# Optimization experiments

Measured on AMD Instinct MI355X. Metric: run time of the kernel, lower is better.

Reference implementation:

```python
import jax, jax.numpy as jnp
import numpy as np
import math

B_SZ, T, D_IN, D_OUT, N = 8, 4096, 128, 128, 256
MAX_PHASE, RMIN, RMAX = math.pi, 0.0, 1.0


def setup_inputs() -> dict:
    key = jax.random.key(0)
    ks = jax.random.split(key, 9)
    x = jax.random.normal(ks[0], (B_SZ, T, D_IN), dtype=jnp.float32)
    # lambda parameterization exactly as in LRU.__init__
    u1 = jax.random.uniform(ks[1], (N,), minval=1e-4, maxval=1.0)
    u2 = jax.random.uniform(ks[2], (N,), minval=1e-4, maxval=1.0)
    nu_log = jnp.log(-0.5 * jnp.log(u1 * (RMAX + RMIN) * (RMAX - RMIN) + RMIN ** 2))
    theta_log = jnp.log(MAX_PHASE * u2)
    lam_abs = jnp.exp(-jnp.exp(nu_log))
    gamma_log = jnp.log(jnp.sqrt(1.0 - jnp.square(lam_abs)))
    B_re = jax.random.normal(ks[3], (N, D_IN)) / math.sqrt(2 * D_IN)
    B_im = jax.random.normal(ks[4], (N, D_IN)) / math.sqrt(2 * D_IN)
    C_re = jax.random.normal(ks[5], (D_OUT, N)) / math.sqrt(N)
    C_im = jax.random.normal(ks[6], (D_OUT, N)) / math.sqrt(N)
    D = jax.random.normal(ks[7], (D_OUT, D_IN)) / math.sqrt(D_IN)
    return {"x": x, "nu_log": nu_log, "theta_log": theta_log, "gamma_log": gamma_log,
            "B_re": B_re, "B_im": B_im, "C_re": C_re, "C_im": C_im, "D": D}


def _binary_op_diag(e1, e2):
    a1, b1 = e1
    a2, b2 = e2
    return a1 * a2, a2 * b1 + b2


def reference(x, nu_log, theta_log, gamma_log, B_re, B_im, C_re, C_im, D):
    # ss_params()
    lam_abs = jnp.exp(-jnp.exp(nu_log))
    phase = jnp.exp(theta_log)
    lam = (lam_abs * jnp.cos(phase) + 1j * (lam_abs * jnp.sin(phase))).astype(jnp.complex64)  # [N]
    gammas = jnp.exp(gamma_log)[:, None]
    Bc = (gammas * (B_re + 1j * B_im)).astype(jnp.complex64)  # [N, D_IN]
    Cc = (C_re + 1j * C_im).astype(jnp.complex64)             # [D_OUT, N]
    # diagonal complex linear recurrence via associative scan over time
    Bu = x.astype(Bc.dtype) @ Bc.T                            # [B, T, N] complex
    lam_el = jnp.broadcast_to(lam, Bu.shape)                  # [B, T, N]
    _, states = jax.lax.associative_scan(_binary_op_diag, (lam_el, Bu), axis=1)
    y = jnp.real(states @ Cc.T) + x @ D.T                     # [B, T, D_OUT]
    return y
```

## Files before the change

### kernel.cpp

```cpp
#include <hip/hip_runtime.h>
#include <math.h>

#define B_SZ 8
#define T_LEN 4096
#define D_IN 128
#define D_OUT 128
#define N_ST 256
#define BT (B_SZ * T_LEN)
#define CHUNK 64
#define NCHUNK (T_LEN / CHUNK)
#define NBLK (B_SZ * NCHUNK)

typedef __attribute__((ext_vector_type(8))) short short8;
typedef __attribute__((ext_vector_type(4))) float f32x4;
typedef unsigned int uint;
typedef unsigned short ushort;

static __device__ __forceinline__ short f2bf(float f) {
  union { float f; uint u; } v; v.f = f;
  uint r = v.u + 0x7FFFu + ((v.u >> 16) & 1u);
  return (short)(r >> 16);
}
static __device__ __forceinline__ float bf2f(uint h) {
  union { uint u; float f; } v; v.u = h << 16;
  return v.f;
}
static __device__ __forceinline__ uint pack2(float a, float b) {
  return (uint)(ushort)f2bf(a) | ((uint)(ushort)f2bf(b) << 16);
}

__global__ __launch_bounds__(256) void k0_setup(
    const float* __restrict__ x,
    const float* __restrict__ nu_log, const float* __restrict__ theta_log,
    const float* __restrict__ gamma_log,
    const float* __restrict__ B_re, const float* __restrict__ B_im,
    const float* __restrict__ C_re, const float* __restrict__ C_im,
    const float* __restrict__ Dm,
    short* __restrict__ Wf1, short* __restrict__ Wf2,
    float2* __restrict__ lampow2, short* __restrict__ xbf) {
  int blk = blockIdx.x;
  if (blk < 320) {
    int idx = blk * 256 + threadIdx.x;
    if (idx < 16 * 512 * 8) {
      int j = idx & 7, col = (idx >> 3) & 511, kg = idx >> 12;
      int k = kg * 8 + j;
      int n = col >> 1, ri = col & 1;
      float g = expf(gamma_log[n]);
      float v = g * (ri ? B_im[n * D_IN + k] : B_re[n * D_IN + k]);
      Wf1[idx] = f2bf(v);
    }
    if (idx < 80 * 128 * 8) {
      int j = idx & 7, d = (idx >> 3) & 127, kg = idx >> 10;
      int k = kg * 8 + j;
      float v;
      if (k < 512) {
        int n = k >> 1;
        v = (k & 1) ? -C_im[d * N_ST + n] : C_re[d * N_ST + n];
      } else {
        v = Dm[d * D_IN + (k - 512)];
      }
      Wf2[idx] = f2bf(v);
    }
  } else if (blk < 385) {
    int j = blk - 320;
    int n = threadIdx.x;
    float e_nu = expf(nu_log[n]);
    float phase = expf(theta_log[n]);
    float r = expf(-(float)j * e_nu);
    float a = (float)j * phase;
    float2 v; v.x = r * cosf(a); v.y = r * sinf(a);
    lampow2[j * N_ST + n] = v;
  } else {
    size_t i = (size_t)(blk - 385) * 256 + threadIdx.x;
    const float4* x4 = (const float4*)x;
    float4 a = x4[2 * i], b = x4[2 * i + 1];
    uint4 u;
    u.x = pack2(a.x, a.y); u.y = pack2(a.z, a.w);
    u.z = pack2(b.x, b.y); u.w = pack2(b.z, b.w);
    ((uint4*)xbf)[i] = u;
  }
}

__global__ __launch_bounds__(256, 2) void kA(
    const short* __restrict__ xbf, const short* __restrict__ Wf1,
    const float2* __restrict__ lampow2,
    uint* __restrict__ states, float2* __restrict__ E) {
  __shared__ short bu[64 * 520];

  int bc = blockIdx.x;
  size_t row0 = (size_t)bc * CHUNK;
  int tid = threadIdx.x;
  int lane = tid & 63, w = tid >> 6;
  int m = lane & 15, q = lane >> 4;

  f32x4 acc[32];
#pragma unroll
  for (int ct = 0; ct < 32; ++ct) acc[ct] = (f32x4){0.f, 0.f, 0.f, 0.f};

  const short* xrow = xbf + (row0 + 16 * w + m) * D_IN;

  for (int ks = 0; ks < 4; ++ks) {
    short8 af = *(const short8*)(xrow + 32 * ks + 8 * q);
    const short* wbase = Wf1 + ((size_t)(4 * ks + q) * 512 + m) * 8;
#pragma unroll
    for (int ct = 0; ct < 32; ++ct) {
      short8 bf = *(const short8*)(wbase + 16 * ct * 8);
      acc[ct] = __builtin_amdgcn_mfma_f32_16x16x32_bf16(af, bf, acc[ct], 0, 0, 0);
    }
  }

#pragma unroll
  for (int ct = 0; ct < 32; ++ct) {
#pragma unroll
    for (int r = 0; r < 4; ++r) {
      bu[(16 * w + 4 * q + r) * 520 + 16 * ct + m] = f2bf(acc[ct][r]);
    }
  }
  __syncthreads();

  int n = tid;
  float2 lam = lampow2[N_ST + n];
  float sre = 0.f, sim = 0.f;
  uint* sg = states + row0 * N_ST + n;
  for (int j = 0; j < CHUNK; ++j) {
    uint p = ((const uint*)(bu + j * 520))[n];
    float br = bf2f(p & 0xffffu), bi = bf2f(p >> 16);
    float nr = fmaf(lam.x, sre, fmaf(-lam.y, sim, br));
    float ni = fmaf(lam.x, sim, fmaf(lam.y, sre, bi));
    sre = nr; sim = ni;
    sg[(size_t)j * N_ST] = pack2(sre, sim);
  }
  float2 e; e.x = sre; e.y = sim;
  E[bc * N_ST + n] = e;
}

__global__ __launch_bounds__(256) void kB(
    const float2* __restrict__ E, const float2* __restrict__ lampow2,
    float2* __restrict__ P) {
  __shared__ float2 Es[NCHUNK * N_ST];

  int b = blockIdx.x;
  int tid = threadIdx.x;

  const float4* src = (const float4*)(E + (size_t)b * NCHUNK * N_ST);
  float4* dst = (float4*)Es;
#pragma unroll
  for (int it = 0; it < (NCHUNK * N_ST / 2) / 256; ++it) {
    dst[it * 256 + tid] = src[it * 256 + tid];
  }
  __syncthreads();

  int n = tid;
  float2 lamL = lampow2[CHUNK * N_ST + n];
  float cre = 0.f, cim = 0.f;
  for (int c = 0; c < NCHUNK; ++c) {
    size_t i = ((size_t)b * NCHUNK + c) * N_ST + n;
    float2 pv; pv.x = cre; pv.y = cim;
    P[i] = pv;
    float2 e = Es[c * N_ST + n];
    float nre = fmaf(lamL.x, cre, fmaf(-lamL.y, cim, e.x));
    float nim = fmaf(lamL.x, cim, fmaf(lamL.y, cre, e.y));
    cre = nre; cim = nim;
  }
}

__global__ __launch_bounds__(256, 4) void kC(
    const short* __restrict__ xbf, const uint* __restrict__ states,
    const float2* __restrict__ P, const float2* __restrict__ lampow2,
    const short* __restrict__ Wf2, float* __restrict__ y) {
  __shared__ short As[32 * 640];

  int blk = blockIdx.x;
  int bc = blk >> 1;
  int j0 = (blk & 1) * 32;
  size_t row0 = (size_t)blk * 32;
  int tid = threadIdx.x;
  int n4 = tid & 63, rblk = tid >> 6;

  float4 pA = *(const float4*)(P + (size_t)bc * N_ST + 4 * n4);
  float4 pB = *(const float4*)(P + (size_t)bc * N_ST + 4 * n4 + 2);

  {
    int kxp = tid & 63, r0 = tid >> 6;
    int k = 512 + 2 * kxp;
    int g = k >> 3, koff = k & 7;
    for (int rr = 0; rr < 8; ++rr) {
      int row = r0 * 8 + rr;
      uint xv = *(const uint*)(xbf + (row0 + row) * D_IN + 2 * kxp);
      int gp = (g & ~7) | ((g + row) & 7);
      *(uint*)(As + row * 640 + gp * 8 + koff) = xv;
    }
  }

  {
#pragma unroll
    for (int rr = 0; rr < 8; ++rr) {
      int row = rblk * 8 + rr;
      int j = j0 + row;
      uint4 sp = *(const uint4*)(states + ((row0 + row) * N_ST + 4 * n4));
      float4 lpa = *(const float4*)(lampow2 + ((size_t)(j + 1) * N_ST + 4 * n4));
      float4 lpb = *(const float4*)(lampow2 + ((size_t)(j + 1) * N_ST + 4 * n4 + 2));
      uint4 outv;
      {
        float sr = bf2f(sp.x & 0xffffu) + lpa.x * pA.x - lpa.y * pA.y;
        float si = bf2f(sp.x >> 16)     + lpa.x * pA.y + lpa.y * pA.x;
        outv.x = pack2(sr, si);
      }
      {
        float sr = bf2f(sp.y & 0xffffu) + lpa.z * pA.z - lpa.w * pA.w;
        float si = bf2f(sp.y >> 16)     + lpa.z * pA.w + lpa.w * pA.z;
        outv.y = pack2(sr, si);
      }
      {
        float sr = bf2f(sp.z & 0xffffu) + lpb.x * pB.x - lpb.y * pB.y;
        float si = bf2f(sp.z >> 16)     + lpb.x * pB.y + lpb.y * pB.x;
        outv.z = pack2(sr, si);
      }
      {
        float sr = bf2f(sp.w & 0xffffu) + lpb.z * pB.z - lpb.w * pB.w;
        float si = bf2f(sp.w >> 16)     + lpb.z * pB.w + lpb.w * pB.z;
        outv.w = pack2(sr, si);
      }
      int g = n4;
      int gp = (g & ~7) | ((g + row) & 7);
      *(uint4*)(As + row * 640 + gp * 8) = outv;
    }
  }
  __syncthreads();

  int lane = tid & 63, w = tid >> 6;
  int m = lane & 15, q = lane >> 4;

  f32x4 acc[2][2];
#pragma unroll
  for (int rt = 0; rt < 2; ++rt)
#pragma unroll
    for (int ci = 0; ci < 2; ++ci) acc[rt][ci] = (f32x4){0.f, 0.f, 0.f, 0.f};

  for (int ks = 0; ks < 20; ++ks) {
    int g = 4 * ks + q;
    int gp = (g & ~7) | ((g + m) & 7);
    short8 af0 = *(const short8*)(As + m * 640 + gp * 8);
    short8 af1 = *(const short8*)(As + (16 + m) * 640 + gp * 8);
    const short* wbase = Wf2 + ((size_t)g * 128 + m) * 8;
#pragma unroll
    for (int ci = 0; ci < 2; ++ci) {
      int ctg = 2 * w + ci;
      short8 bf = *(const short8*)(wbase + 16 * ctg * 8);
      acc[0][ci] = __builtin_amdgcn_mfma_f32_16x16x32_bf16(af0, bf, acc[0][ci], 0, 0, 0);
      acc[1][ci] = __builtin_amdgcn_mfma_f32_16x16x32_bf16(af1, bf, acc[1][ci], 0, 0, 0);
    }
  }

#pragma unroll
  for (int ci = 0; ci < 2; ++ci) {
    int ctg = 2 * w + ci;
#pragma unroll
    for (int rt = 0; rt < 2; ++rt) {
#pragma unroll
      for (int r = 0; r < 4; ++r) {
        y[(row0 + 16 * rt + 4 * q + r) * D_OUT + 16 * ctg + m] = acc[rt][ci][r];
      }
    }
  }
}

extern "C" void kernel_launch(void* const* d_in, const int* in_sizes, int n_in,
                              void* d_out, int out_size, void* d_ws, size_t ws_size,
                              hipStream_t stream) {
  const float* x         = (const float*)d_in[0];
  const float* nu_log    = (const float*)d_in[1];
  const float* theta_log = (const float*)d_in[2];
  const float* gamma_log = (const float*)d_in[3];
  const float* B_re      = (const float*)d_in[4];
  const float* B_im      = (const float*)d_in[5];
  const float* C_re      = (const float*)d_in[6];
  const float* C_im      = (const float*)d_in[7];
  const float* Dm        = (const float*)d_in[8];
  float* y = (float*)d_out;

  char* wp = (char*)d_ws;
  float2* lampow2 = (float2*)wp; wp += (size_t)(CHUNK + 1) * N_ST * sizeof(float2);
  short*  Wf1     = (short*)wp;  wp += (size_t)16 * 512 * 8 * sizeof(short);
  short*  Wf2     = (short*)wp;  wp += (size_t)80 * 128 * 8 * sizeof(short);
  float2* E       = (float2*)wp; wp += (size_t)NBLK * N_ST * sizeof(float2);
  float2* P       = (float2*)wp; wp += (size_t)NBLK * N_ST * sizeof(float2);
  short*  xbf     = (short*)wp;  wp += (size_t)BT * D_IN * sizeof(short);
  uint*   states  = (uint*)wp;   wp += (size_t)BT * N_ST * sizeof(uint);

  hipLaunchKernelGGL(k0_setup, dim3(385 + BT * D_IN / 8 / 256), dim3(256), 0, stream,
                     x, nu_log, theta_log, gamma_log, B_re, B_im, C_re, C_im,
                     Dm, Wf1, Wf2, lampow2, xbf);
  hipLaunchKernelGGL(kA, dim3(NBLK), dim3(256), 0, stream,
                     xbf, Wf1, lampow2, states, E);
  hipLaunchKernelGGL(kB, dim3(B_SZ), dim3(256), 0, stream,
                     E, lampow2, P);
  hipLaunchKernelGGL(kC, dim3(2 * NBLK), dim3(256), 0, stream,
                     xbf, states, P, lampow2, Wf2, y);
}
```

Before: 129.6 us.

## Recompute chunk-local scan in output kernel instead of storing states

```diff
diff --git a/kernel.cpp b/kernel.cpp
--- a/kernel.cpp
+++ b/kernel.cpp
@@ -83,8 +83,7 @@
 
 __global__ __launch_bounds__(256, 2) void kA(
     const short* __restrict__ xbf, const short* __restrict__ Wf1,
-    const float2* __restrict__ lampow2,
-    uint* __restrict__ states, float2* __restrict__ E) {
+    const float2* __restrict__ lampow2, float2* __restrict__ E) {
   __shared__ short bu[64 * 520];
 
   int bc = blockIdx.x;
@@ -121,14 +120,12 @@
   int n = tid;
   float2 lam = lampow2[N_ST + n];
   float sre = 0.f, sim = 0.f;
-  uint* sg = states + row0 * N_ST + n;
   for (int j = 0; j < CHUNK; ++j) {
     uint p = ((const uint*)(bu + j * 520))[n];
     float br = bf2f(p & 0xffffu), bi = bf2f(p >> 16);
     float nr = fmaf(lam.x, sre, fmaf(-lam.y, sim, br));
     float ni = fmaf(lam.x, sim, fmaf(lam.y, sre, bi));
     sre = nr; sim = ni;
-    sg[(size_t)j * N_ST] = pack2(sre, sim);
   }
   float2 e; e.x = sre; e.y = sim;
   E[bc * N_ST + n] = e;
@@ -164,102 +161,110 @@
   }
 }
 
-__global__ __launch_bounds__(256, 4) void kC(
-    const short* __restrict__ xbf, const uint* __restrict__ states,
+__global__ __launch_bounds__(256, 1) void kC(
+    const short* __restrict__ xbf, const short* __restrict__ Wf1,
     const float2* __restrict__ P, const float2* __restrict__ lampow2,
     const short* __restrict__ Wf2, float* __restrict__ y) {
-  __shared__ short As[32 * 640];
-
-  int blk = blockIdx.x;
-  int bc = blk >> 1;
-  int j0 = (blk & 1) * 32;
-  size_t row0 = (size_t)blk * 32;
+  __shared__ short bu[64 * 520];
+  __shared__ short As[64 * 640];
+
+  int bc = blockIdx.x;
+  size_t row0 = (size_t)bc * CHUNK;
   int tid = threadIdx.x;
-  int n4 = tid & 63, rblk = tid >> 6;
-
-  float4 pA = *(const float4*)(P + (size_t)bc * N_ST + 4 * n4);
-  float4 pB = *(const float4*)(P + (size_t)bc * N_ST + 4 * n4 + 2);
+  int lane = tid & 63, w = tid >> 6;
+  int m = lane & 15, q = lane >> 4;
+
+  f32x4 acc[32];
+#pragma unroll
+  for (int ct = 0; ct < 32; ++ct) acc[ct] = (f32x4){0.f, 0.f, 0.f, 0.f};
+
+  const short* xrow = xbf + (row0 + 16 * w + m) * D_IN;
+
+  for (int ks = 0; ks < 4; ++ks) {
+    short8 af = *(const short8*)(xrow + 32 * ks + 8 * q);
+    const short* wbase = Wf1 + ((size_t)(4 * ks + q) * 512 + m) * 8;
+#pragma unroll
+    for (int ct = 0; ct < 32; ++ct) {
+      short8 bf = *(const short8*)(wbase + 16 * ct * 8);
+      acc[ct] = __builtin_amdgcn_mfma_f32_16x16x32_bf16(af, bf, acc[ct], 0, 0, 0);
+    }
+  }
+
+#pragma unroll
+  for (int ct = 0; ct < 32; ++ct) {
+#pragma unroll
+    for (int r = 0; r < 4; ++r) {
+      bu[(16 * w + 4 * q + r) * 520 + 16 * ct + m] = f2bf(acc[ct][r]);
+    }
+  }
 
   {
     int kxp = tid & 63, r0 = tid >> 6;
     int k = 512 + 2 * kxp;
     int g = k >> 3, koff = k & 7;
-    for (int rr = 0; rr < 8; ++rr) {
-      int row = r0 * 8 + rr;
+    for (int rr = 0; rr < 16; ++rr) {
+      int row = r0 * 16 + rr;
       uint xv = *(const uint*)(xbf + (row0 + row) * D_IN + 2 * kxp);
       int gp = (g & ~7) | ((g + row) & 7);
       *(uint*)(As + row * 640 + gp * 8 + koff) = xv;
     }
   }
+  __syncthreads();
 
   {
-#pragma unroll
-    for (int rr = 0; rr < 8; ++rr) {
-      int row = rblk * 8 + rr;
-      int j = j0 + row;
-      uint4 sp = *(const uint4*)(states + ((row0 + row) * N_ST + 4 * n4));
-      float4 lpa = *(const float4*)(lampow2 + ((size_t)(j + 1) * N_ST + 4 * n4));
-      float4 lpb = *(const float4*)(lampow2 + ((size_t)(j + 1) * N_ST + 4 * n4 + 2));
-      uint4 outv;
-      {
-        float sr = bf2f(sp.x & 0xffffu) + lpa.x * pA.x - lpa.y * pA.y;
-        float si = bf2f(sp.x >> 16)     + lpa.x * pA.y + lpa.y * pA.x;
-        outv.x = pack2(sr, si);
-      }
-      {
-        float sr = bf2f(sp.y & 0xffffu) + lpa.z * pA.z - lpa.w * pA.w;
-        float si = bf2f(sp.y >> 16)     + lpa.z * pA.w + lpa.w * pA.z;
-        outv.y = pack2(sr, si);
-      }
-      {
-        float sr = bf2f(sp.z & 0xffffu) + lpb.x * pB.x - lpb.y * pB.y;
-        float si = bf2f(sp.z >> 16)     + lpb.x * pB.y + lpb.y * pB.x;
-        outv.z = pack2(sr, si);
-      }
-      {
-        float sr = bf2f(sp.w & 0xffffu) + lpb.z * pB.z - lpb.w * pB.w;
-        float si = bf2f(sp.w >> 16)     + lpb.z * pB.w + lpb.w * pB.z;
-        outv.w = pack2(sr, si);
-      }
-      int g = n4;
-      int gp = (g & ~7) | ((g + row) & 7);
-      *(uint4*)(As + row * 640 + gp * 8) = outv;
+    int n = tid;
+    float2 lam = lampow2[N_ST + n];
+    float2 pc = P[(size_t)bc * N_ST + n];
+    float sre = 0.f, sim = 0.f;
+    int g2 = n >> 2, koff2 = (2 * n) & 7;
+    for (int j = 0; j < CHUNK; ++j) {
+      uint p = ((const uint*)(bu + j * 520))[n];
+      float br = bf2f(p & 0xffffu), bi = bf2f(p >> 16);
+      float nr = fmaf(lam.x, sre, fmaf(-lam.y, sim, br));
+      float ni = fmaf(lam.x, sim, fmaf(lam.y, sre, bi));
+      sre = nr; sim = ni;
+      uint sp = pack2(sre, sim);
+      float2 lp = lampow2[(size_t)(j + 1) * N_ST + n];
+      float sr = bf2f(sp & 0xffffu) + lp.x * pc.x - lp.y * pc.y;
+      float si = bf2f(sp >> 16)     + lp.x * pc.y + lp.y * pc.x;
+      int gp = (g2 & ~7) | ((g2 + j) & 7);
+      *(uint*)(As + j * 640 + gp * 8 + koff2) = pack2(sr, si);
     }
   }
   __syncthreads();
 
-  int lane = tid & 63, w = tid >> 6;
-  int m = lane & 15, q = lane >> 4;
-
-  f32x4 acc[2][2];
+  int rw = w & 1, ch = w >> 1;
+
+  f32x4 acc2[2][4];
 #pragma unroll
   for (int rt = 0; rt < 2; ++rt)
 #pragma unroll
-    for (int ci = 0; ci < 2; ++ci) acc[rt][ci] = (f32x4){0.f, 0.f, 0.f, 0.f};
+    for (int ci = 0; ci < 4; ++ci) acc2[rt][ci] = (f32x4){0.f, 0.f, 0.f, 0.f};
 
   for (int ks = 0; ks < 20; ++ks) {
     int g = 4 * ks + q;
-    int gp = (g & ~7) | ((g + m) & 7);
-    short8 af0 = *(const short8*)(As + m * 640 + gp * 8);
-    short8 af1 = *(const short8*)(As + (16 + m) * 640 + gp * 8);
+    int arow0 = 32 * rw + m;
+    int gp = (g & ~7) | ((g + arow0) & 7);
+    short8 af0 = *(const short8*)(As + arow0 * 640 + gp * 8);
+    short8 af1 = *(const short8*)(As + (arow0 + 16) * 640 + gp * 8);
     const short* wbase = Wf2 + ((size_t)g * 128 + m) * 8;
 #pragma unroll
-    for (int ci = 0; ci < 2; ++ci) {
-      int ctg = 2 * w + ci;
+    for (int ci = 0; ci < 4; ++ci) {
+      int ctg = 4 * ch + ci;
       short8 bf = *(const short8*)(wbase + 16 * ctg * 8);
-      acc[0][ci] = __builtin_amdgcn_mfma_f32_16x16x32_bf16(af0, bf, acc[0][ci], 0, 0, 0);
-      acc[1][ci] = __builtin_amdgcn_mfma_f32_16x16x32_bf16(af1, bf, acc[1][ci], 0, 0, 0);
-    }
-  }
-
-#pragma unroll
-  for (int ci = 0; ci < 2; ++ci) {
-    int ctg = 2 * w + ci;
+      acc2[0][ci] = __builtin_amdgcn_mfma_f32_16x16x32_bf16(af0, bf, acc2[0][ci], 0, 0, 0);
+      acc2[1][ci] = __builtin_amdgcn_mfma_f32_16x16x32_bf16(af1, bf, acc2[1][ci], 0, 0, 0);
+    }
+  }
+
+#pragma unroll
+  for (int ci = 0; ci < 4; ++ci) {
+    int ctg = 4 * ch + ci;
 #pragma unroll
     for (int rt = 0; rt < 2; ++rt) {
 #pragma unroll
       for (int r = 0; r < 4; ++r) {
-        y[(row0 + 16 * rt + 4 * q + r) * D_OUT + 16 * ctg + m] = acc[rt][ci][r];
+        y[(row0 + 32 * rw + 16 * rt + 4 * q + r) * D_OUT + 16 * ctg + m] = acc2[rt][ci][r];
       }
     }
   }
@@ -286,15 +291,14 @@
   float2* E       = (float2*)wp; wp += (size_t)NBLK * N_ST * sizeof(float2);
   float2* P       = (float2*)wp; wp += (size_t)NBLK * N_ST * sizeof(float2);
   short*  xbf     = (short*)wp;  wp += (size_t)BT * D_IN * sizeof(short);
-  uint*   states  = (uint*)wp;   wp += (size_t)BT * N_ST * sizeof(uint);
 
   hipLaunchKernelGGL(k0_setup, dim3(385 + BT * D_IN / 8 / 256), dim3(256), 0, stream,
                      x, nu_log, theta_log, gamma_log, B_re, B_im, C_re, C_im,
                      Dm, Wf1, Wf2, lampow2, xbf);
   hipLaunchKernelGGL(kA, dim3(NBLK), dim3(256), 0, stream,
-                     xbf, Wf1, lampow2, states, E);
+                     xbf, Wf1, lampow2, E);
   hipLaunchKernelGGL(kB, dim3(B_SZ), dim3(256), 0, stream,
                      E, lampow2, P);
-  hipLaunchKernelGGL(kC, dim3(2 * NBLK), dim3(256), 0, stream,
-                     xbf, states, P, lampow2, Wf2, y);
-}
+  hipLaunchKernelGGL(kC, dim3(NBLK), dim3(256), 0, stream,
+                     xbf, Wf1, P, lampow2, Wf2, y);
+}
```

New measurement: 157.1 us. 21.2% more time.

## Fuse x conversion and cross-chunk carry into consumer kernels, coalesce state stores

Applied to the files above, without the earlier changes.

```diff
diff --git a/kernel.cpp b/kernel.cpp
--- a/kernel.cpp
+++ b/kernel.cpp
@@ -28,16 +28,23 @@
 static __device__ __forceinline__ uint pack2(float a, float b) {
   return (uint)(ushort)f2bf(a) | ((uint)(ushort)f2bf(b) << 16);
 }
-
-__global__ __launch_bounds__(256) void k0_setup(
-    const float* __restrict__ x,
+static __device__ __forceinline__ short8 cvt8(const float* __restrict__ p) {
+  float4 a = *(const float4*)p;
+  float4 b = *(const float4*)(p + 4);
+  union { short8 s; uint4 u; } r;
+  r.u.x = pack2(a.x, a.y); r.u.y = pack2(a.z, a.w);
+  r.u.z = pack2(b.x, b.y); r.u.w = pack2(b.z, b.w);
+  return r.s;
+}
+
+__global__ __launch_bounds__(256) void k0w(
     const float* __restrict__ nu_log, const float* __restrict__ theta_log,
     const float* __restrict__ gamma_log,
     const float* __restrict__ B_re, const float* __restrict__ B_im,
     const float* __restrict__ C_re, const float* __restrict__ C_im,
     const float* __restrict__ Dm,
     short* __restrict__ Wf1, short* __restrict__ Wf2,
-    float2* __restrict__ lampow2, short* __restrict__ xbf) {
+    float2* __restrict__ lampow2) {
   int blk = blockIdx.x;
   if (blk < 320) {
     int idx = blk * 256 + threadIdx.x;
@@ -61,7 +68,7 @@
       }
       Wf2[idx] = f2bf(v);
     }
-  } else if (blk < 385) {
+  } else {
     int j = blk - 320;
     int n = threadIdx.x;
     float e_nu = expf(nu_log[n]);
@@ -70,19 +77,11 @@
     float a = (float)j * phase;
     float2 v; v.x = r * cosf(a); v.y = r * sinf(a);
     lampow2[j * N_ST + n] = v;
-  } else {
-    size_t i = (size_t)(blk - 385) * 256 + threadIdx.x;
-    const float4* x4 = (const float4*)x;
-    float4 a = x4[2 * i], b = x4[2 * i + 1];
-    uint4 u;
-    u.x = pack2(a.x, a.y); u.y = pack2(a.z, a.w);
-    u.z = pack2(b.x, b.y); u.w = pack2(b.z, b.w);
-    ((uint4*)xbf)[i] = u;
   }
 }
 
 __global__ __launch_bounds__(256, 2) void kA(
-    const short* __restrict__ xbf, const short* __restrict__ Wf1,
+    const float* __restrict__ x, const short* __restrict__ Wf1,
     const float2* __restrict__ lampow2,
     uint* __restrict__ states, float2* __restrict__ E) {
   __shared__ short bu[64 * 520];
@@ -97,10 +96,10 @@
 #pragma unroll
   for (int ct = 0; ct < 32; ++ct) acc[ct] = (f32x4){0.f, 0.f, 0.f, 0.f};
 
-  const short* xrow = xbf + (row0 + 16 * w + m) * D_IN;
+  const float* xrowf = x + (row0 + 16 * w + m) * D_IN;
 
   for (int ks = 0; ks < 4; ++ks) {
-    short8 af = *(const short8*)(xrow + 32 * ks + 8 * q);
+    short8 af = cvt8(xrowf + 32 * ks + 8 * q);
     const short* wbase = Wf1 + ((size_t)(4 * ks + q) * 512 + m) * 8;
 #pragma unroll
     for (int ct = 0; ct < 32; ++ct) {
@@ -118,67 +117,72 @@
   }
   __syncthreads();
 
-  int n = tid;
-  float2 lam = lampow2[N_ST + n];
-  float sre = 0.f, sim = 0.f;
-  uint* sg = states + row0 * N_ST + n;
-  for (int j = 0; j < CHUNK; ++j) {
-    uint p = ((const uint*)(bu + j * 520))[n];
-    float br = bf2f(p & 0xffffu), bi = bf2f(p >> 16);
-    float nr = fmaf(lam.x, sre, fmaf(-lam.y, sim, br));
-    float ni = fmaf(lam.x, sim, fmaf(lam.y, sre, bi));
-    sre = nr; sim = ni;
-    sg[(size_t)j * N_ST] = pack2(sre, sim);
-  }
-  float2 e; e.x = sre; e.y = sim;
-  E[bc * N_ST + n] = e;
-}
-
-__global__ __launch_bounds__(256) void kB(
+  {
+    int n = tid;
+    float2 lam = lampow2[N_ST + n];
+    float sre = 0.f, sim = 0.f;
+    for (int j = 0; j < CHUNK; ++j) {
+      uint p = ((const uint*)(bu + j * 520))[n];
+      float br = bf2f(p & 0xffffu), bi = bf2f(p >> 16);
+      float nr = fmaf(lam.x, sre, fmaf(-lam.y, sim, br));
+      float ni = fmaf(lam.x, sim, fmaf(lam.y, sre, bi));
+      sre = nr; sim = ni;
+      ((uint*)(bu + j * 520))[n] = pack2(sre, sim);
+    }
+    float2 e; e.x = sre; e.y = sim;
+    E[bc * N_ST + n] = e;
+  }
+  __syncthreads();
+
+  for (int i = 0; i < 16; ++i) {
+    int idx = i * 256 + tid;
+    int row = idx >> 6;
+    int c4  = idx & 63;
+    ((uint4*)(states + (size_t)(row0 + row) * N_ST))[c4] =
+        *(const uint4*)((const uint*)(bu + row * 520) + 4 * c4);
+  }
+}
+
+__global__ __launch_bounds__(256, 4) void kC(
+    const float* __restrict__ x, const uint* __restrict__ states,
     const float2* __restrict__ E, const float2* __restrict__ lampow2,
-    float2* __restrict__ P) {
-  __shared__ float2 Es[NCHUNK * N_ST];
-
-  int b = blockIdx.x;
-  int tid = threadIdx.x;
-
-  const float4* src = (const float4*)(E + (size_t)b * NCHUNK * N_ST);
-  float4* dst = (float4*)Es;
-#pragma unroll
-  for (int it = 0; it < (NCHUNK * N_ST / 2) / 256; ++it) {
-    dst[it * 256 + tid] = src[it * 256 + tid];
-  }
-  __syncthreads();
-
-  int n = tid;
-  float2 lamL = lampow2[CHUNK * N_ST + n];
-  float cre = 0.f, cim = 0.f;
-  for (int c = 0; c < NCHUNK; ++c) {
-    size_t i = ((size_t)b * NCHUNK + c) * N_ST + n;
-    float2 pv; pv.x = cre; pv.y = cim;
-    P[i] = pv;
-    float2 e = Es[c * N_ST + n];
-    float nre = fmaf(lamL.x, cre, fmaf(-lamL.y, cim, e.x));
-    float nim = fmaf(lamL.x, cim, fmaf(lamL.y, cre, e.y));
-    cre = nre; cim = nim;
-  }
-}
-
-__global__ __launch_bounds__(256, 4) void kC(
-    const short* __restrict__ xbf, const uint* __restrict__ states,
-    const float2* __restrict__ P, const float2* __restrict__ lampow2,
     const short* __restrict__ Wf2, float* __restrict__ y) {
   __shared__ short As[32 * 640];
+  __shared__ float2 Pl[N_ST];
 
   int blk = blockIdx.x;
   int bc = blk >> 1;
-  int j0 = (blk & 1) * 32;
   size_t row0 = (size_t)blk * 32;
   int tid = threadIdx.x;
   int n4 = tid & 63, rblk = tid >> 6;
 
-  float4 pA = *(const float4*)(P + (size_t)bc * N_ST + 4 * n4);
-  float4 pB = *(const float4*)(P + (size_t)bc * N_ST + 4 * n4 + 2);
+  {
+    int b = bc >> 6, c = bc & 63;
+    int n = tid;
+    float2 lamL = lampow2[CHUNK * N_ST + n];
+    const float2* Eb = E + (size_t)(b << 6) * N_ST;
+    float cre = 0.f, cim = 0.f;
+    for (int t = 0; t < NCHUNK; t += 8) {
+      if (t >= c) break;
+      float2 eb[8];
+#pragma unroll
+      for (int u = 0; u < 8; ++u)
+        if (t + u < c) eb[u] = Eb[(size_t)(t + u) * N_ST + n];
+#pragma unroll
+      for (int u = 0; u < 8; ++u)
+        if (t + u < c) {
+          float nre = fmaf(lamL.x, cre, fmaf(-lamL.y, cim, eb[u].x));
+          float nim = fmaf(lamL.x, cim, fmaf(lamL.y, cre, eb[u].y));
+          cre = nre; cim = nim;
+        }
+    }
+    float2 pv; pv.x = cre; pv.y = cim;
+    Pl[n] = pv;
+  }
+  __syncthreads();
+
+  float4 pA = *(const float4*)(&Pl[4 * n4]);
+  float4 pB = *(const float4*)(&Pl[4 * n4 + 2]);
 
   {
     int kxp = tid & 63, r0 = tid >> 6;
@@ -186,13 +190,15 @@
     int g = k >> 3, koff = k & 7;
     for (int rr = 0; rr < 8; ++rr) {
       int row = r0 * 8 + rr;
-      uint xv = *(const uint*)(xbf + (row0 + row) * D_IN + 2 * kxp);
+      const float* xp = x + (row0 + row) * D_IN + 2 * kxp;
+      uint xv = pack2(xp[0], xp[1]);
       int gp = (g & ~7) | ((g + row) & 7);
       *(uint*)(As + row * 640 + gp * 8 + koff) = xv;
     }
   }
 
   {
+    int j0 = (blk & 1) * 32;
 #pragma unroll
     for (int rr = 0; rr < 8; ++rr) {
       int row = rblk * 8 + rr;
@@ -284,17 +290,13 @@
   short*  Wf1     = (short*)wp;  wp += (size_t)16 * 512 * 8 * sizeof(short);
   short*  Wf2     = (short*)wp;  wp += (size_t)80 * 128 * 8 * sizeof(short);
   float2* E       = (float2*)wp; wp += (size_t)NBLK * N_ST * sizeof(float2);
-  float2* P       = (float2*)wp; wp += (size_t)NBLK * N_ST * sizeof(float2);
-  short*  xbf     = (short*)wp;  wp += (size_t)BT * D_IN * sizeof(short);
   uint*   states  = (uint*)wp;   wp += (size_t)BT * N_ST * sizeof(uint);
 
-  hipLaunchKernelGGL(k0_setup, dim3(385 + BT * D_IN / 8 / 256), dim3(256), 0, stream,
-                     x, nu_log, theta_log, gamma_log, B_re, B_im, C_re, C_im,
-                     Dm, Wf1, Wf2, lampow2, xbf);
+  hipLaunchKernelGGL(k0w, dim3(385), dim3(256), 0, stream,
+                     nu_log, theta_log, gamma_log, B_re, B_im, C_re, C_im,
+                     Dm, Wf1, Wf2, lampow2);
   hipLaunchKernelGGL(kA, dim3(NBLK), dim3(256), 0, stream,
-                     xbf, Wf1, lampow2, states, E);
-  hipLaunchKernelGGL(kB, dim3(B_SZ), dim3(256), 0, stream,
-                     E, lampow2, P);
+                     x, Wf1, lampow2, states, E);
   hipLaunchKernelGGL(kC, dim3(2 * NBLK), dim3(256), 0, stream,
-                     xbf, states, P, lampow2, Wf2, y);
-}
+                     x, states, E, lampow2, Wf2, y);
+}
```

After: 130.9 us. No clear change (+1.0%).
